# Kernel tuning notes

Hardware: AMD Instinct MI355X
Metric: run time of the kernel (lower is better)

Reference implementation:

```python
import jax, jax.numpy as jnp
import numpy as np

NUM_HEADS = 6

def setup_inputs() -> dict:
    key = jax.random.key(0)
    k1, k2, k3, k4 = jax.random.split(key, 4)
    B, T, C = 128, 256, 384
    s = 1.0 / np.sqrt(C)
    return {
        'x': jax.random.normal(k1, (B, T, C), dtype=jnp.float32),
        'Wq': jax.random.normal(k2, (C, C), dtype=jnp.float32) * s,
        'Wk': jax.random.normal(k3, (C, C), dtype=jnp.float32) * s,
        'Wv': jax.random.normal(k4, (C, C), dtype=jnp.float32) * s,
    }

def reference(x, Wq, Wk, Wv):
    B, T, C = x.shape
    H = NUM_HEADS
    d = C // H
    # projections (bias-free Linear), split into heads
    q = (x @ Wq).reshape(B, T, H, d)
    k = (x @ Wk).reshape(B, T, H, d)
    v = (x @ Wv).reshape(B, T, H, d)
    # NOTE: original scales by 1/sqrt(C), not 1/sqrt(head_dim)
    scale = 1.0 / jnp.sqrt(jnp.asarray(C, dtype=x.dtype))
    att = jnp.einsum('bqhd,bkhd->bhqk', q, k) * scale  # [B,H,T,T]
    causal = jnp.tril(jnp.ones((T, T), dtype=bool))
    att = jnp.where(causal, att, -jnp.inf)
    att = jax.nn.softmax(att, axis=-1)
    # dropout is identity in eval/deterministic mode
    out = jnp.einsum('bhqk,bkhd->bqhd', att, v)  # [B,T,H,d]
    return out.reshape(B, T, C)
```

## Files before the change

### kernel.cpp

```cpp
#include <hip/hip_runtime.h>


typedef unsigned short u16;
typedef float f32x4 __attribute__((ext_vector_type(4)));
typedef short s16x8 __attribute__((ext_vector_type(8)));
typedef u16 u16x4 __attribute__((ext_vector_type(4)));

static constexpr int BB = 128;
static constexpr int TT = 256;
static constexpr int CC = 384;
static constexpr int HH = 6;
static constexpr int DD = 64;
static constexpr int MM = BB * TT;

static constexpr size_t WTOFF = 0;
static constexpr size_t XOFF  = (size_t)3 * CC * CC;

static constexpr float CSC = 0.07362242194579907f;

__device__ __forceinline__ u16 f2bf(float f) {
  unsigned u = __float_as_uint(f);
  u += 0x7fffu + ((u >> 16) & 1u);
  return (u16)(u >> 16);
}

__device__ __forceinline__ unsigned cvtpk(float lo, float hi) {
  unsigned r;
  asm("v_cvt_pk_bf16_f32 %0, %1, %2" : "=v"(r) : "v"(lo), "v"(hi));
  return r;
}

__device__ __forceinline__ void g2l16(const u16* g, u16* l) {
  __builtin_amdgcn_global_load_lds(
      (const __attribute__((address_space(1))) u16*)g,
      (__attribute__((address_space(3))) u16*)l, 16, 0, 0);
}

__global__ void prep(const float* __restrict__ X, const float* __restrict__ Wq,
                     const float* __restrict__ Wk, const float* __restrict__ Wv,
                     u16* __restrict__ ws) {
  int bx = blockIdx.x;
  if (bx < 6144) {
    size_t i = (size_t)(bx * 256 + threadIdx.x) * 8;
    f32x4 a0 = *(const f32x4*)(X + i);
    f32x4 a1 = *(const f32x4*)(X + i + 4);
    s16x8 ab;
#pragma unroll
    for (int j = 0; j < 4; ++j) { ab[j] = (short)f2bf(a0[j]); ab[4 + j] = (short)f2bf(a1[j]); }
    *(s16x8*)(ws + XOFF + i) = ab;
  } else {
    __shared__ u16 Lt[64][66];
    int j = bx - 6144;
    int z = j / 36, t = j % 36, ti = t / 6, tj = t % 6;
    const float* W = (z == 0) ? Wq : (z == 1) ? Wk : Wv;
    const float sc = (z == 0) ? CSC : 1.0f;
    u16* WT = ws + WTOFF + (size_t)z * CC * CC;
    const int rl = threadIdx.x >> 4;
    const int cl = (threadIdx.x & 15) * 4;
#pragma unroll
    for (int it = 0; it < 4; ++it) {
      int r = it * 16 + rl;
      f32x4 v = *(const f32x4*)(W + (size_t)(ti * 64 + r) * CC + tj * 64 + cl);
#pragma unroll
      for (int q = 0; q < 4; ++q) Lt[r][cl + q] = f2bf(v[q] * sc);
    }
    __syncthreads();
#pragma unroll
    for (int it = 0; it < 4; ++it) {
      int n = it * 16 + rl;
      u16x4 o;
#pragma unroll
      for (int q = 0; q < 4; ++q) o[q] = Lt[cl + q][n];
      *(u16x4*)(WT + (size_t)(tj * 64 + n) * CC + ti * 64 + cl) = o;
    }
  }
}

__global__ __launch_bounds__(512, 2) void fused(const u16* __restrict__ ws,
                                                float* __restrict__ out) {
  const int bid = blockIdx.x;
  const int xc = bid & 7;
  const int g5 = bid >> 3;
  const int b = xc * 16 + g5 / 6;
  const int h = g5 % 6;

  __shared__ u16 X2[2][256][64];
  __shared__ u16 W2[2][192][64];
  __shared__ u16 VTs[64][256];

  const int tid = threadIdx.x;
  const int lane = tid & 63;
  const int w = tid >> 6;
  const int quad = lane >> 4;
  const int col = lane & 15;

  const u16* Xg = ws + XOFF + (size_t)b * TT * CC;
  const u16* Wg = ws + WTOFF;

  const int rl = lane >> 3;
  const int gb = (lane & 7) ^ rl;

  const int wm = (w >> 1) * 64;
  const int wn = (w & 1) * 96;

  auto stage = [&](int kt) {
    int bufi = kt & 1;
#pragma unroll
    for (int i = 0; i < 4; ++i) {
      int r0 = w * 32 + i * 8;
      g2l16(Xg + (size_t)(r0 + rl) * CC + kt * 64 + gb * 8, &X2[bufi][r0][0]);
    }
#pragma unroll
    for (int i = 0; i < 3; ++i) {
      int r0 = w * 24 + i * 8;
      int rr = r0 + rl;
      int z = rr >> 6, nn = rr & 63;
      g2l16(Wg + (size_t)(z * CC + h * DD + nn) * CC + kt * 64 + gb * 8,
            &W2[bufi][r0][0]);
    }
  };

  f32x4 acc[4][6] = {};

  stage(0);
  __syncthreads();

  for (int kt = 0; kt < 6; ++kt) {
    const int bufi = kt & 1;
    if (kt < 5) stage(kt + 1);

    s16x8 af[4][2], bf[6][2];
#pragma unroll
    for (int mt = 0; mt < 4; ++mt)
#pragma unroll
      for (int ks = 0; ks < 2; ++ks)
        af[mt][ks] = *(const s16x8*)(&X2[bufi][wm + mt * 16 + col]
                                        [(((ks * 4 + quad) ^ (col & 7)) * 8)]);
#pragma unroll
    for (int nt = 0; nt < 6; ++nt)
#pragma unroll
      for (int ks = 0; ks < 2; ++ks)
        bf[nt][ks] = *(const s16x8*)(&W2[bufi][wn + nt * 16 + col]
                                        [(((ks * 4 + quad) ^ (col & 7)) * 8)]);

    __builtin_amdgcn_s_setprio(1);
#pragma unroll
    for (int ks = 0; ks < 2; ++ks)
#pragma unroll
      for (int mt = 0; mt < 4; ++mt)
#pragma unroll
        for (int nt = 0; nt < 6; ++nt)
          acc[mt][nt] = __builtin_amdgcn_mfma_f32_16x16x32_bf16(
              af[mt][ks], bf[nt][ks], acc[mt][nt], 0, 0, 0);
    __builtin_amdgcn_s_setprio(0);

    __syncthreads();
  }

  u16* Qb  = &X2[0][0][0];
  u16* KsB = &X2[1][0][0];
#pragma unroll
  for (int mt = 0; mt < 4; ++mt) {
    int tokb = wm + mt * 16 + quad * 4;
#pragma unroll
    for (int nt = 0; nt < 6; ++nt) {
      int gn = wn + nt * 16 + col;
      unsigned u01 = cvtpk(acc[mt][nt][0], acc[mt][nt][1]);
      unsigned u23 = cvtpk(acc[mt][nt][2], acc[mt][nt][3]);
      if (gn < 128) {
        u16* dst = (gn < 64) ? Qb : KsB;
        int d = gn & 63;
        dst[(tokb + 0) * 64 + (d ^ (((tokb + 0) & 7) << 3))] = (u16)u01;
        dst[(tokb + 1) * 64 + (d ^ (((tokb + 1) & 7) << 3))] = (u16)(u01 >> 16);
        dst[(tokb + 2) * 64 + (d ^ (((tokb + 2) & 7) << 3))] = (u16)u23;
        dst[(tokb + 3) * 64 + (d ^ (((tokb + 3) & 7) << 3))] = (u16)(u23 >> 16);
      } else {
        int d = gn - 128;
        *(uint2*)((u16*)VTs + d * 256 + (tokb ^ ((d & 15) << 3))) =
            make_uint2(u01, u23);
      }
    }
  }
  __syncthreads();

  const int g0 = w, g1 = 15 - w;
  const int k0max = g0 >> 2, k1max = g1 >> 2;
  const int qq0 = (g0 & 3) * 16 + col;
  const int qq1 = (g1 & 3) * 16 + col;
  u16* PsA = (u16*)W2 + w * 2048;
  u16* PsB = PsA + 1024;

  s16x8 qf[2][2];
  {
    int qr0 = g0 * 16 + col, qr1 = g1 * 16 + col;
#pragma unroll
    for (int ks = 0; ks < 2; ++ks) {
      qf[0][ks] = *(const s16x8*)(Qb + qr0 * 64 + (((ks * 4 + quad) ^ (col & 7)) * 8));
      qf[1][ks] = *(const s16x8*)(Qb + qr1 * 64 + (((ks * 4 + quad) ^ (col & 7)) * 8));
    }
  }

  f32x4 o[2][4] = {};
  float mst[2] = {-1.0e30f, -1.0e30f}, lst[2] = {0.0f, 0.0f};

  auto sm = [&](f32x4 (&s)[4], bool diag, int qq, float& m, float& l,
                u16* Ps, bool& deferred) -> float {
    float mx[4];
#pragma unroll
    for (int nt = 0; nt < 4; ++nt) {
      if (diag) {
#pragma unroll
        for (int r = 0; r < 4; ++r)
          if ((nt * 16 + quad * 4 + r) > qq) s[nt][r] = -1.0e30f;
      }
      mx[nt] = fmaxf(fmaxf(s[nt][0], s[nt][1]), fmaxf(s[nt][2], s[nt][3]));
    }
    float rmax = fmaxf(fmaxf(mx[0], mx[1]), fmaxf(mx[2], mx[3]));
    rmax = fmaxf(rmax, __shfl_xor(rmax, 16));
    rmax = fmaxf(rmax, __shfl_xor(rmax, 32));

    deferred = __all(rmax - m <= 8.0f);
    float alpha = 1.0f;
    if (!deferred) {
      float mn = fmaxf(m, rmax);
      alpha = exp2f(m - mn);
      m = mn;
    }
    float lsum = 0.0f;
#pragma unroll
    for (int nt = 0; nt < 4; ++nt) {
      float p0 = exp2f(s[nt][0] - m), p1 = exp2f(s[nt][1] - m);
      float p2 = exp2f(s[nt][2] - m), p3 = exp2f(s[nt][3] - m);
      *(uint2*)(Ps + col * 64 + ((nt * 16 + quad * 4) ^ ((col & 7) << 3))) =
          make_uint2(cvtpk(p0, p1), cvtpk(p2, p3));
      lsum += (p0 + p1) + (p2 + p3);
    }
    l = l * alpha + lsum;
    return alpha;
  };

  for (int kt = 0; kt <= k1max; ++kt) {
    const bool both = (kt <= k0max);

    s16x8 kf[4][2], vf[4][2];
#pragma unroll
    for (int nt = 0; nt < 4; ++nt)
#pragma unroll
      for (int ks = 0; ks < 2; ++ks) {
        int key = kt * 64 + nt * 16 + col;
        kf[nt][ks] = *(const s16x8*)(KsB + key * 64 +
                                     (((ks * 4 + quad) ^ (col & 7)) * 8));
        int d = nt * 16 + col;
        vf[nt][ks] = *(const s16x8*)((const u16*)VTs + d * 256 +
                     ((kt * 64 + ks * 32 + quad * 8) ^ ((d & 15) << 3)));
      }

    f32x4 sA[4] = {}, sB[4] = {};
    __builtin_amdgcn_s_setprio(1);
    if (both) {
#pragma unroll
      for (int ks = 0; ks < 2; ++ks)
#pragma unroll
        for (int nt = 0; nt < 4; ++nt)
          sA[nt] = __builtin_amdgcn_mfma_f32_16x16x32_bf16(kf[nt][ks], qf[0][ks],
                                                           sA[nt], 0, 0, 0);
    }
#pragma unroll
    for (int ks = 0; ks < 2; ++ks)
#pragma unroll
      for (int nt = 0; nt < 4; ++nt)
        sB[nt] = __builtin_amdgcn_mfma_f32_16x16x32_bf16(kf[nt][ks], qf[1][ks],
                                                         sB[nt], 0, 0, 0);
    __builtin_amdgcn_s_setprio(0);

    bool dfA = true, dfB;
    float aA = 1.0f, aB;
    if (both) aA = sm(sA, kt == k0max, qq0, mst[0], lst[0], PsA, dfA);
    aB = sm(sB, kt == k1max, qq1, mst[1], lst[1], PsB, dfB);

    if (both && !dfA) {
#pragma unroll
      for (int dt = 0; dt < 4; ++dt)
#pragma unroll
        for (int r = 0; r < 4; ++r) o[0][dt][r] *= aA;
    }
    if (!dfB) {
#pragma unroll
      for (int dt = 0; dt < 4; ++dt)
#pragma unroll
        for (int r = 0; r < 4; ++r) o[1][dt][r] *= aB;
    }

    asm volatile("s_waitcnt lgkmcnt(0)" ::: "memory");

    s16x8 pfA[2], pfB[2];
    if (both) {
#pragma unroll
      for (int ks = 0; ks < 2; ++ks)
        pfA[ks] = *(const s16x8*)(PsA + col * 64 +
                                  ((ks * 32 + quad * 8) ^ ((col & 7) << 3)));
    }
#pragma unroll
    for (int ks = 0; ks < 2; ++ks)
      pfB[ks] = *(const s16x8*)(PsB + col * 64 +
                                ((ks * 32 + quad * 8) ^ ((col & 7) << 3)));

    __builtin_amdgcn_s_setprio(1);
    if (both) {
#pragma unroll
      for (int ks = 0; ks < 2; ++ks)
#pragma unroll
        for (int dt = 0; dt < 4; ++dt)
          o[0][dt] = __builtin_amdgcn_mfma_f32_16x16x32_bf16(vf[dt][ks], pfA[ks],
                                                             o[0][dt], 0, 0, 0);
    }
#pragma unroll
    for (int ks = 0; ks < 2; ++ks)
#pragma unroll
      for (int dt = 0; dt < 4; ++dt)
        o[1][dt] = __builtin_amdgcn_mfma_f32_16x16x32_bf16(vf[dt][ks], pfB[ks],
                                                           o[1][dt], 0, 0, 0);
    __builtin_amdgcn_s_setprio(0);
  }

#pragma unroll
  for (int gi = 0; gi < 2; ++gi) {
    int g = gi ? g1 : g0;
    float l = lst[gi];
    l += __shfl_xor(l, 16);
    l += __shfl_xor(l, 32);
    float inv = 1.0f / l;
    int q = g * 16 + col;
#pragma unroll
    for (int dt = 0; dt < 4; ++dt) {
      f32x4 res;
#pragma unroll
      for (int r = 0; r < 4; ++r) res[r] = o[gi][dt][r] * inv;
      *(f32x4*)(out + (size_t)(b * TT + q) * CC + h * DD + dt * 16 + quad * 4) = res;
    }
  }
}

extern "C" void kernel_launch(void* const* d_in, const int* in_sizes, int n_in,
                              void* d_out, int out_size, void* d_ws, size_t ws_size,
                              hipStream_t stream) {
  const float* x  = (const float*)d_in[0];
  const float* wq = (const float*)d_in[1];
  const float* wk = (const float*)d_in[2];
  const float* wv = (const float*)d_in[3];
  u16* ws  = (u16*)d_ws;
  float* out = (float*)d_out;

  prep<<<dim3(6144 + 108), 256, 0, stream>>>(x, wq, wk, wv, ws);
  fused<<<dim3(BB * HH), 512, 0, stream>>>(ws, out);
}
```

Measured before the change: 153.8 us.

## Fuse X bf16 conversion into projection GEMM, load operands directly from global

```diff
diff --git a/kernel.cpp b/kernel.cpp
--- a/kernel.cpp
+++ b/kernel.cpp
@@ -11,10 +11,6 @@
 static constexpr int CC = 384;
 static constexpr int HH = 6;
 static constexpr int DD = 64;
-static constexpr int MM = BB * TT;
-
-static constexpr size_t WTOFF = 0;
-static constexpr size_t XOFF  = (size_t)3 * CC * CC;
 
 static constexpr float CSC = 0.07362242194579907f;
 
@@ -30,53 +26,42 @@
   return r;
 }
 
-__device__ __forceinline__ void g2l16(const u16* g, u16* l) {
-  __builtin_amdgcn_global_load_lds(
-      (const __attribute__((address_space(1))) u16*)g,
-      (__attribute__((address_space(3))) u16*)l, 16, 0, 0);
-}
-
-__global__ void prep(const float* __restrict__ X, const float* __restrict__ Wq,
-                     const float* __restrict__ Wk, const float* __restrict__ Wv,
-                     u16* __restrict__ ws) {
-  int bx = blockIdx.x;
-  if (bx < 6144) {
-    size_t i = (size_t)(bx * 256 + threadIdx.x) * 8;
-    f32x4 a0 = *(const f32x4*)(X + i);
-    f32x4 a1 = *(const f32x4*)(X + i + 4);
-    s16x8 ab;
-#pragma unroll
-    for (int j = 0; j < 4; ++j) { ab[j] = (short)f2bf(a0[j]); ab[4 + j] = (short)f2bf(a1[j]); }
-    *(s16x8*)(ws + XOFF + i) = ab;
-  } else {
-    __shared__ u16 Lt[64][66];
-    int j = bx - 6144;
-    int z = j / 36, t = j % 36, ti = t / 6, tj = t % 6;
-    const float* W = (z == 0) ? Wq : (z == 1) ? Wk : Wv;
-    const float sc = (z == 0) ? CSC : 1.0f;
-    u16* WT = ws + WTOFF + (size_t)z * CC * CC;
-    const int rl = threadIdx.x >> 4;
-    const int cl = (threadIdx.x & 15) * 4;
-#pragma unroll
-    for (int it = 0; it < 4; ++it) {
-      int r = it * 16 + rl;
-      f32x4 v = *(const f32x4*)(W + (size_t)(ti * 64 + r) * CC + tj * 64 + cl);
-#pragma unroll
-      for (int q = 0; q < 4; ++q) Lt[r][cl + q] = f2bf(v[q] * sc);
-    }
-    __syncthreads();
-#pragma unroll
-    for (int it = 0; it < 4; ++it) {
-      int n = it * 16 + rl;
-      u16x4 o;
-#pragma unroll
-      for (int q = 0; q < 4; ++q) o[q] = Lt[cl + q][n];
-      *(u16x4*)(WT + (size_t)(tj * 64 + n) * CC + ti * 64 + cl) = o;
-    }
-  }
-}
-
-__global__ __launch_bounds__(512, 2) void fused(const u16* __restrict__ ws,
+__device__ __forceinline__ s16x8 pack4(unsigned a, unsigned b, unsigned c, unsigned d) {
+  union { unsigned u[4]; s16x8 v; } t;
+  t.u[0] = a; t.u[1] = b; t.u[2] = c; t.u[3] = d;
+  return t.v;
+}
+
+__global__ void prep_w(const float* __restrict__ Wq, const float* __restrict__ Wk,
+                       const float* __restrict__ Wv, u16* __restrict__ ws) {
+  __shared__ u16 Lt[64][66];
+  int j = blockIdx.x;
+  int z = j / 36, t = j % 36, ti = t / 6, tj = t % 6;
+  const float* W = (z == 0) ? Wq : (z == 1) ? Wk : Wv;
+  const float sc = (z == 0) ? CSC : 1.0f;
+  u16* WT = ws + (size_t)z * CC * CC;
+  const int rl = threadIdx.x >> 4;
+  const int cl = (threadIdx.x & 15) * 4;
+#pragma unroll
+  for (int it = 0; it < 4; ++it) {
+    int r = it * 16 + rl;
+    f32x4 v = *(const f32x4*)(W + (size_t)(ti * 64 + r) * CC + tj * 64 + cl);
+#pragma unroll
+    for (int q = 0; q < 4; ++q) Lt[r][cl + q] = f2bf(v[q] * sc);
+  }
+  __syncthreads();
+#pragma unroll
+  for (int it = 0; it < 4; ++it) {
+    int n = it * 16 + rl;
+    u16x4 o;
+#pragma unroll
+    for (int q = 0; q < 4; ++q) o[q] = Lt[cl + q][n];
+    *(u16x4*)(WT + (size_t)(tj * 64 + n) * CC + ti * 64 + cl) = o;
+  }
+}
+
+__global__ __launch_bounds__(512, 2) void fused(const float* __restrict__ X,
+                                                const u16* __restrict__ ws,
                                                 float* __restrict__ out) {
   const int bid = blockIdx.x;
   const int xc = bid & 7;
@@ -84,9 +69,10 @@
   const int b = xc * 16 + g5 / 6;
   const int h = g5 % 6;
 
-  __shared__ u16 X2[2][256][64];
-  __shared__ u16 W2[2][192][64];
+  __shared__ u16 Qs[256][64];
+  __shared__ u16 Ks[256][64];
   __shared__ u16 VTs[64][256];
+  __shared__ u16 Ps[8][2048];
 
   const int tid = threadIdx.x;
   const int lane = tid & 63;
@@ -94,56 +80,42 @@
   const int quad = lane >> 4;
   const int col = lane & 15;
 
-  const u16* Xg = ws + XOFF + (size_t)b * TT * CC;
-  const u16* Wg = ws + WTOFF;
-
-  const int rl = lane >> 3;
-  const int gb = (lane & 7) ^ rl;
-
   const int wm = (w >> 1) * 64;
   const int wn = (w & 1) * 96;
 
-  auto stage = [&](int kt) {
-    int bufi = kt & 1;
-#pragma unroll
-    for (int i = 0; i < 4; ++i) {
-      int r0 = w * 32 + i * 8;
-      g2l16(Xg + (size_t)(r0 + rl) * CC + kt * 64 + gb * 8, &X2[bufi][r0][0]);
-    }
-#pragma unroll
-    for (int i = 0; i < 3; ++i) {
-      int r0 = w * 24 + i * 8;
-      int rr = r0 + rl;
-      int z = rr >> 6, nn = rr & 63;
-      g2l16(Wg + (size_t)(z * CC + h * DD + nn) * CC + kt * 64 + gb * 8,
-            &W2[bufi][r0][0]);
-    }
-  };
+  const float* Xg = X + (size_t)b * TT * CC;
+
+  const float* arow[4];
+#pragma unroll
+  for (int mt = 0; mt < 4; ++mt) arow[mt] = Xg + (size_t)(wm + mt * 16 + col) * CC;
+  const u16* brow[6];
+#pragma unroll
+  for (int nt = 0; nt < 6; ++nt) {
+    int gn = wn + nt * 16 + col;
+    brow[nt] = ws + (size_t)((gn >> 6) * CC + h * DD + (gn & 63)) * CC;
+  }
 
   f32x4 acc[4][6] = {};
 
-  stage(0);
-  __syncthreads();
-
+#pragma unroll
   for (int kt = 0; kt < 6; ++kt) {
-    const int bufi = kt & 1;
-    if (kt < 5) stage(kt + 1);
-
+    const int d0 = kt * 64 + quad * 8;
     s16x8 af[4][2], bf[6][2];
 #pragma unroll
     for (int mt = 0; mt < 4; ++mt)
 #pragma unroll
+      for (int ks = 0; ks < 2; ++ks) {
+        f32x4 x0 = *(const f32x4*)(arow[mt] + d0 + ks * 32);
+        f32x4 x1 = *(const f32x4*)(arow[mt] + d0 + ks * 32 + 4);
+        af[mt][ks] = pack4(cvtpk(x0[0], x0[1]), cvtpk(x0[2], x0[3]),
+                           cvtpk(x1[0], x1[1]), cvtpk(x1[2], x1[3]));
+      }
+#pragma unroll
+    for (int nt = 0; nt < 6; ++nt)
+#pragma unroll
       for (int ks = 0; ks < 2; ++ks)
-        af[mt][ks] = *(const s16x8*)(&X2[bufi][wm + mt * 16 + col]
-                                        [(((ks * 4 + quad) ^ (col & 7)) * 8)]);
-#pragma unroll
-    for (int nt = 0; nt < 6; ++nt)
-#pragma unroll
-      for (int ks = 0; ks < 2; ++ks)
-        bf[nt][ks] = *(const s16x8*)(&W2[bufi][wn + nt * 16 + col]
-                                        [(((ks * 4 + quad) ^ (col & 7)) * 8)]);
-
-    __builtin_amdgcn_s_setprio(1);
+        bf[nt][ks] = *(const s16x8*)(brow[nt] + d0 + ks * 32);
+
 #pragma unroll
     for (int ks = 0; ks < 2; ++ks)
 #pragma unroll
@@ -152,13 +124,10 @@
         for (int nt = 0; nt < 6; ++nt)
           acc[mt][nt] = __builtin_amdgcn_mfma_f32_16x16x32_bf16(
               af[mt][ks], bf[nt][ks], acc[mt][nt], 0, 0, 0);
-    __builtin_amdgcn_s_setprio(0);
-
-    __syncthreads();
-  }
-
-  u16* Qb  = &X2[0][0][0];
-  u16* KsB = &X2[1][0][0];
+  }
+
+  u16* Qb  = &Qs[0][0];
+  u16* KsB = &Ks[0][0];
 #pragma unroll
   for (int mt = 0; mt < 4; ++mt) {
     int tokb = wm + mt * 16 + quad * 4;
@@ -187,7 +156,7 @@
   const int k0max = g0 >> 2, k1max = g1 >> 2;
   const int qq0 = (g0 & 3) * 16 + col;
   const int qq1 = (g1 & 3) * 16 + col;
-  u16* PsA = (u16*)W2 + w * 2048;
+  u16* PsA = &Ps[w][0];
   u16* PsB = PsA + 1024;
 
   s16x8 qf[2][2];
@@ -204,7 +173,7 @@
   float mst[2] = {-1.0e30f, -1.0e30f}, lst[2] = {0.0f, 0.0f};
 
   auto sm = [&](f32x4 (&s)[4], bool diag, int qq, float& m, float& l,
-                u16* Ps, bool& deferred) -> float {
+                u16* Ps_, bool& deferred) -> float {
     float mx[4];
 #pragma unroll
     for (int nt = 0; nt < 4; ++nt) {
@@ -231,7 +200,7 @@
     for (int nt = 0; nt < 4; ++nt) {
       float p0 = exp2f(s[nt][0] - m), p1 = exp2f(s[nt][1] - m);
       float p2 = exp2f(s[nt][2] - m), p3 = exp2f(s[nt][3] - m);
-      *(uint2*)(Ps + col * 64 + ((nt * 16 + quad * 4) ^ ((col & 7) << 3))) =
+      *(uint2*)(Ps_ + col * 64 + ((nt * 16 + quad * 4) ^ ((col & 7) << 3))) =
           make_uint2(cvtpk(p0, p1), cvtpk(p2, p3));
       lsum += (p0 + p1) + (p2 + p3);
     }
@@ -351,6 +320,6 @@
   u16* ws  = (u16*)d_ws;
   float* out = (float*)d_out;
 
-  prep<<<dim3(6144 + 108), 256, 0, stream>>>(x, wq, wk, wv, ws);
-  fused<<<dim3(BB * HH), 512, 0, stream>>>(ws, out);
-}
+  prep_w<<<dim3(108), 256, 0, stream>>>(wq, wk, wv, ws);
+  fused<<<dim3(BB * HH), 512, 0, stream>>>(x, ws, out);
+}
```

Measured after the change: 237.3 us. 54.3% more time.
